# Kernel tuning notes

Hardware: AMD Instinct MI355X
Metric: run time of the kernel (lower is better)

Reference implementation:

```python
import jax, jax.numpy as jnp
import numpy as np

B, L, D = 8, 2048, 10
MIN_INTENSITY = 1e-12


def setup_inputs() -> dict:
    key = jax.random.key(0)
    k1, k2, k3, k4, k5 = jax.random.split(key, 5)
    # strictly increasing event times per sequence in [0, ~100)
    time_points = jnp.sort(jax.random.uniform(k1, (B, L), dtype=jnp.float32) * 100.0, axis=1)
    T = time_points[:, -1] + 1.0  # observation horizon per batch element
    event_types = jax.random.randint(k2, (B, L), 0, D)  # all valid (no -1 padding)
    mu_raw = jax.random.normal(k3, (D,), dtype=jnp.float32)
    log_alpha = jax.random.normal(k4, (D, D), dtype=jnp.float32) - 2.0
    log_beta = jax.random.normal(k5, (D, D), dtype=jnp.float32)
    return {"time_points": time_points, "T": T, "mu_raw": mu_raw,
            "log_alpha": log_alpha, "log_beta": log_beta, "event_types": event_types}


def reference(time_points, T, mu_raw, log_alpha, log_beta, event_types):
    sp = jax.nn.softplus
    mu, alpha, beta = sp(mu_raw), sp(log_alpha), sp(log_beta)  # (D,), (D,D), (D,D)
    e = event_types                      # (B, L)
    valid = e >= 0                       # padding marked with -1
    e_safe = jnp.where(valid, e, 0)

    # ---- positive (event) log-likelihood: O(L^2) pairwise exp-decay sums ----
    td = time_points[:, :, None] - time_points[:, None, :]        # (B, L, L) t_i - t_j
    a = alpha[e_safe[:, :, None], e_safe[:, None, :]]             # (B, L, L)
    b = beta[e_safe[:, :, None], e_safe[:, None, :]]
    expo = jnp.clip(-b * td, -20.0, 0.0)                          # clamp as in source
    inter = a * b * jnp.exp(expo)
    tri = jnp.tril(jnp.ones((L, L), dtype=bool), -1)              # strictly past events
    vmask = valid[:, :, None] & valid[:, None, :]
    inter = jnp.where(tri[None, :, :] & vmask, inter, 0.0)
    lam = mu[e_safe] * valid.astype(mu.dtype) + inter.sum(-1)     # (B, L) intensities
    logl = jnp.where(valid, jnp.log(jnp.clip(lam, MIN_INTENSITY, None)), 0.0)
    pos = logl.sum(-1)                                            # (B,)
    n_valid = valid.sum(-1)
    pos = jnp.where(n_valid == 0, 0.0, pos)

    # ---- compensator: cumulative intensity integral over [0, T] ----
    dt = jnp.where(valid, T[:, None] - time_points, 0.0)          # (B, L)
    ae = alpha[:, e_safe]                                         # (D, B, L)
    be = beta[:, e_safe]
    contrib = ae * (1.0 - jnp.exp(-be * dt[None, :, :]))
    contrib = jnp.where(valid[None, :, :], contrib, 0.0)
    integral = mu[:, None] * T[None, :] + contrib.sum(-1)         # (D, B)

    return pos - integral.sum(0)                                  # (B,) log-likelihood
```

## Files before the change

### kernel.cpp

```cpp
#include <hip/hip_runtime.h>
#include <math.h>

#define NB 8
#define L 2048
#define ND 10
#define NSLICE 32
#define JS 64
#define IT 256
#define TABR 11
#define LOG2E 1.4426950408889634f
#define LN2   0.6931471805599453f
#define CLIP2 (-28.853900817779268f)

#if __has_builtin(__builtin_amdgcn_exp2f)
#define EXP2F(x) __builtin_amdgcn_exp2f(x)
#else
#define EXP2F(x) exp2f(x)
#endif
#if __has_builtin(__builtin_amdgcn_logf)
#define LOGNF(x) (LN2 * __builtin_amdgcn_logf(x))
#else
#define LOGNF(x) logf(x)
#endif

__device__ __forceinline__ float softplus(float x) {
    return (x > 20.0f) ? x : log1pf(expf(x));
}

__global__ __launch_bounds__(256) void hawkes_pairs(
    const float* __restrict__ tp, const int* __restrict__ et,
    const float* __restrict__ la, const float* __restrict__ lb,
    float* __restrict__ part)
{
    __shared__ float2 tab[TABR * ND];
    __shared__ int2   js[JS];
    const int tid = threadIdx.x;

    if (tid < ND * ND) {
        const float a  = softplus(la[tid]);
        const float bb = softplus(lb[tid]);
        const int ei = tid / ND, ej = tid % ND;
        tab[ej * ND + ei] = make_float2(a * bb, bb * LOG2E);
    } else if (tid < ND * ND + ND) {
        tab[ND * ND + (tid - ND * ND)] = make_float2(0.0f, 0.0f);
    }

    const int bx = blockIdx.x;
    const int b  = blockIdx.y;
    int k = 7;
    while (k > 0 && bx < 2 * k * (k + 1)) --k;
    const int s = bx - 2 * k * (k + 1);
    const int jbase = s * JS;
    const int i = k * IT + tid;

    if (tid < JS) {
        const int   ejraw = et[b * L + jbase + tid];
        const float tj    = tp[b * L + jbase + tid];
        const int   ejs   = (ejraw >= 0) ? ejraw : ND;
        js[tid] = make_int2(__float_as_int(tj), ejs * (int)(ND * sizeof(float2)));
    }
    __syncthreads();

    const float ti    = tp[b * L + i];
    const int   eiraw = et[b * L + i];
    const bool  vi    = eiraw >= 0;
    const char* tabp  = (const char*)tab + (vi ? eiraw : 0) * (int)sizeof(float2);

    float acc = 0.0f;
    if (jbase < k * IT) {
        #pragma unroll 16
        for (int jj = 0; jj < JS; ++jj) {
            const int2   q = js[jj];
            const float2 p = *(const float2*)(tabp + q.y);
            const float  x = fmaxf(p.y * (__int_as_float(q.x) - ti), CLIP2);
            acc = fmaf(p.x, EXP2F(x), acc);
        }
    } else {
        #pragma unroll 16
        for (int jj = 0; jj < JS; ++jj) {
            const int2   q = js[jj];
            const float2 p = *(const float2*)(tabp + q.y);
            const float  x = fmaxf(p.y * (__int_as_float(q.x) - ti), CLIP2);
            const float  w = (jbase + jj < i) ? p.x : 0.0f;
            acc = fmaf(w, EXP2F(x), acc);
        }
    }
    part[(b * NSLICE + s) * L + i] = vi ? acc : 0.0f;
}

__global__ __launch_bounds__(256) void hawkes_row(
    const float* __restrict__ tp, const float* __restrict__ Tv,
    const float* __restrict__ mu_raw, const float* __restrict__ la,
    const float* __restrict__ lb, const int* __restrict__ et,
    const float* __restrict__ part, float4* __restrict__ rowred)
{
    __shared__ float aT[ND * ND];
    __shared__ float bT[ND * ND];
    __shared__ float mus[ND];
    __shared__ float rp[4], ri[4];
    __shared__ int   rn[4];

    const int tid  = threadIdx.x;
    const int tile = blockIdx.x;
    const int b    = blockIdx.y;
    if (tid < ND * ND) {
        const int d = tid / ND, c = tid % ND;
        aT[c * ND + d] = softplus(la[tid]);
        bT[c * ND + d] = softplus(lb[tid]) * LOG2E;
    }
    if (tid < ND) mus[tid] = softplus(mu_raw[tid]);
    __syncthreads();

    const int   i    = tile * IT + tid;
    const int   eraw = et[b * L + i];
    const float ti   = tp[b * L + i];
    const bool  v    = eraw >= 0;
    const int   es   = v ? eraw : 0;
    const int   ns   = 4 * (tile + 1);
    const float* pp  = part + b * NSLICE * L + i;

    float lam = v ? mus[es] : 0.0f;
    #pragma unroll
    for (int s0 = 0; s0 < NSLICE; s0 += 4) {
        if (s0 < ns) {
            lam += pp[(s0 + 0) * L];
            lam += pp[(s0 + 1) * L];
            lam += pp[(s0 + 2) * L];
            lam += pp[(s0 + 3) * L];
        }
    }

    float pos = 0.0f, integ = 0.0f;
    int nv = 0;
    if (v) {
        pos = LOGNF(fmaxf(lam, 1e-12f));
        nv = 1;
        const float dt = Tv[b] - ti;
        #pragma unroll
        for (int d2 = 0; d2 < ND; ++d2)
            integ += aT[es * ND + d2] * (1.0f - EXP2F(-bT[es * ND + d2] * dt));
    }
    #pragma unroll
    for (int off = 32; off > 0; off >>= 1) {
        pos   += __shfl_down(pos, off);
        integ += __shfl_down(integ, off);
        nv    += __shfl_down(nv, off);
    }
    const int wid = tid >> 6;
    if ((tid & 63) == 0) { rp[wid] = pos; ri[wid] = integ; rn[wid] = nv; }
    __syncthreads();
    if (tid == 0) {
        rowred[b * 8 + tile] = make_float4(rp[0] + rp[1] + rp[2] + rp[3],
                                           ri[0] + ri[1] + ri[2] + ri[3],
                                           (float)(rn[0] + rn[1] + rn[2] + rn[3]),
                                           0.0f);
    }
}

__global__ void hawkes_out(
    const float* __restrict__ Tv, const float* __restrict__ mu_raw,
    const float4* __restrict__ rowred, float* __restrict__ out)
{
    const int b = threadIdx.x;
    float musum = 0.0f;
    #pragma unroll
    for (int d = 0; d < ND; ++d) musum += softplus(mu_raw[d]);
    if (b < NB) {
        float P = 0.0f, I = 0.0f;
        int   N = 0;
        #pragma unroll
        for (int t = 0; t < 8; ++t) {
            const float4 r = rowred[b * 8 + t];
            P += r.x; I += r.y; N += (int)r.z;
        }
        out[b] = ((N == 0) ? 0.0f : P) - (musum * Tv[b] + I);
    }
}

extern "C" void kernel_launch(void* const* d_in, const int* in_sizes, int n_in,
                              void* d_out, int out_size, void* d_ws, size_t ws_size,
                              hipStream_t stream) {
    const float* tp = (const float*)d_in[0];
    const float* Tv = (const float*)d_in[1];
    const float* mu = (const float*)d_in[2];
    const float* la = (const float*)d_in[3];
    const float* lb = (const float*)d_in[4];
    const int*   et = (const int*)d_in[5];
    float* part = (float*)d_ws;
    float4* rowred = (float4*)(part + (0 * NSLICE + 31) * L);
    float* out = (float*)d_out;

    hipLaunchKernelGGL(hawkes_pairs, dim3(144, NB), dim3(256), 0, stream,
                       tp, et, la, lb, part);
    hipLaunchKernelGGL(hawkes_row, dim3(8, NB), dim3(256), 0, stream,
                       tp, Tv, mu, la, lb, et, part, rowred);
    hipLaunchKernelGGL(hawkes_out, dim3(1), dim3(64), 0, stream,
                       Tv, mu, rowred, out);
}
```

Baseline: 79.37 us.

## Fuse three Hawkes kernels into one with last-block-done atomic counters

Merges the pairwise, per-row and final-output kernels into a single launch. Atomic counters pick the last block per row tile to reduce partial sums, and then the last tile overall to write outputs. This removes two kernel launches and the gaps between them, at the cost of a memset, threadfences and atomics in every block.

```diff
diff --git a/kernel.cpp b/kernel.cpp
--- a/kernel.cpp
+++ b/kernel.cpp
@@ -8,6 +8,8 @@
 #define JS 64
 #define IT 256
 #define TABR 11
+#define BLOCKS_PER_B 144
+#define GRID (NB * BLOCKS_PER_B)
 #define LOG2E 1.4426950408889634f
 #define LN2   0.6931471805599453f
 #define CLIP2 (-28.853900817779268f)
@@ -27,14 +29,31 @@
     return (x > 20.0f) ? x : log1pf(expf(x));
 }
 
-__global__ __launch_bounds__(256) void hawkes_pairs(
-    const float* __restrict__ tp, const int* __restrict__ et,
-    const float* __restrict__ la, const float* __restrict__ lb,
-    float* __restrict__ part)
+__global__ __launch_bounds__(256) void hawkes_one(
+    const float* __restrict__ tp, const float* __restrict__ Tv,
+    const float* __restrict__ mu_raw, const float* __restrict__ la,
+    const float* __restrict__ lb, const int* __restrict__ et,
+    float* __restrict__ part, float4* __restrict__ rowred,
+    int* __restrict__ cntT, int* __restrict__ cntD, float* __restrict__ out)
 {
     __shared__ float2 tab[TABR * ND];
     __shared__ int2   js[JS];
+    __shared__ float  aT[ND * ND];
+    __shared__ float  bT[ND * ND];
+    __shared__ float  mus[ND];
+    __shared__ float  rp[4], ri[4];
+    __shared__ int    rn[4];
+    __shared__ int    win;
+
     const int tid = threadIdx.x;
+    const int bx  = blockIdx.x;
+    const int b   = bx / BLOCKS_PER_B;
+    const int r   = bx - b * BLOCKS_PER_B;
+    int k = 7;
+    while (k > 0 && r < 2 * k * (k + 1)) --k;
+    const int s = r - 2 * k * (k + 1);
+    const int jbase = s * JS;
+    const int i = k * IT + tid;
 
     if (tid < ND * ND) {
         const float a  = softplus(la[tid]);
@@ -44,15 +63,6 @@
     } else if (tid < ND * ND + ND) {
         tab[ND * ND + (tid - ND * ND)] = make_float2(0.0f, 0.0f);
     }
-
-    const int bx = blockIdx.x;
-    const int b  = blockIdx.y;
-    int k = 7;
-    while (k > 0 && bx < 2 * k * (k + 1)) --k;
-    const int s = bx - 2 * k * (k + 1);
-    const int jbase = s * JS;
-    const int i = k * IT + tid;
-
     if (tid < JS) {
         const int   ejraw = et[b * L + jbase + tid];
         const float tj    = tp[b * L + jbase + tid];
@@ -86,23 +96,15 @@
         }
     }
     part[(b * NSLICE + s) * L + i] = vi ? acc : 0.0f;
-}
 
-__global__ __launch_bounds__(256) void hawkes_row(
-    const float* __restrict__ tp, const float* __restrict__ Tv,
-    const float* __restrict__ mu_raw, const float* __restrict__ la,
-    const float* __restrict__ lb, const int* __restrict__ et,
-    const float* __restrict__ part, float4* __restrict__ rowred)
-{
-    __shared__ float aT[ND * ND];
-    __shared__ float bT[ND * ND];
-    __shared__ float mus[ND];
-    __shared__ float rp[4], ri[4];
-    __shared__ int   rn[4];
+    const int nslices = 4 * (k + 1);
+    __threadfence();
+    __syncthreads();
+    if (tid == 0) win = (atomicAdd(&cntT[b * 8 + k], 1) == nslices - 1);
+    __syncthreads();
+    if (!win) return;
+    __threadfence();
 
-    const int tid  = threadIdx.x;
-    const int tile = blockIdx.x;
-    const int b    = blockIdx.y;
     if (tid < ND * ND) {
         const int d = tid / ND, c = tid % ND;
         aT[c * ND + d] = softplus(la[tid]);
@@ -111,18 +113,11 @@
     if (tid < ND) mus[tid] = softplus(mu_raw[tid]);
     __syncthreads();
 
-    const int   i    = tile * IT + tid;
-    const int   eraw = et[b * L + i];
-    const float ti   = tp[b * L + i];
-    const bool  v    = eraw >= 0;
-    const int   es   = v ? eraw : 0;
-    const int   ns   = 4 * (tile + 1);
-    const float* pp  = part + b * NSLICE * L + i;
-
-    float lam = v ? mus[es] : 0.0f;
+    const float* pp = part + b * NSLICE * L + i;
+    float lam = vi ? mus[eiraw] : 0.0f;
     #pragma unroll
     for (int s0 = 0; s0 < NSLICE; s0 += 4) {
-        if (s0 < ns) {
+        if (s0 < nslices) {
             lam += pp[(s0 + 0) * L];
             lam += pp[(s0 + 1) * L];
             lam += pp[(s0 + 2) * L];
@@ -132,13 +127,13 @@
 
     float pos = 0.0f, integ = 0.0f;
     int nv = 0;
-    if (v) {
+    if (vi) {
         pos = LOGNF(fmaxf(lam, 1e-12f));
         nv = 1;
         const float dt = Tv[b] - ti;
         #pragma unroll
         for (int d2 = 0; d2 < ND; ++d2)
-            integ += aT[es * ND + d2] * (1.0f - EXP2F(-bT[es * ND + d2] * dt));
+            integ += aT[eiraw * ND + d2] * (1.0f - EXP2F(-bT[eiraw * ND + d2] * dt));
     }
     #pragma unroll
     for (int off = 32; off > 0; off >>= 1) {
@@ -150,30 +145,31 @@
     if ((tid & 63) == 0) { rp[wid] = pos; ri[wid] = integ; rn[wid] = nv; }
     __syncthreads();
     if (tid == 0) {
-        rowred[b * 8 + tile] = make_float4(rp[0] + rp[1] + rp[2] + rp[3],
-                                           ri[0] + ri[1] + ri[2] + ri[3],
-                                           (float)(rn[0] + rn[1] + rn[2] + rn[3]),
-                                           0.0f);
+        rowred[b * 8 + k] = make_float4(rp[0] + rp[1] + rp[2] + rp[3],
+                                        ri[0] + ri[1] + ri[2] + ri[3],
+                                        (float)(rn[0] + rn[1] + rn[2] + rn[3]),
+                                        0.0f);
     }
-}
 
-__global__ void hawkes_out(
-    const float* __restrict__ Tv, const float* __restrict__ mu_raw,
-    const float4* __restrict__ rowred, float* __restrict__ out)
-{
-    const int b = threadIdx.x;
-    float musum = 0.0f;
-    #pragma unroll
-    for (int d = 0; d < ND; ++d) musum += softplus(mu_raw[d]);
-    if (b < NB) {
+    __threadfence();
+    __syncthreads();
+    if (tid == 0) win = (atomicAdd(cntD, 1) == 63);
+    __syncthreads();
+    if (!win) return;
+    __threadfence();
+
+    if (tid < NB) {
+        float musum = 0.0f;
+        #pragma unroll
+        for (int d = 0; d < ND; ++d) musum += softplus(mu_raw[d]);
         float P = 0.0f, I = 0.0f;
         int   N = 0;
         #pragma unroll
         for (int t = 0; t < 8; ++t) {
-            const float4 r = rowred[b * 8 + t];
-            P += r.x; I += r.y; N += (int)r.z;
+            const float4 rr = rowred[tid * 8 + t];
+            P += rr.x; I += rr.y; N += (int)rr.z;
         }
-        out[b] = ((N == 0) ? 0.0f : P) - (musum * Tv[b] + I);
+        out[tid] = ((N == 0) ? 0.0f : P) - (musum * Tv[tid] + I);
     }
 }
 
@@ -186,14 +182,15 @@
     const float* la = (const float*)d_in[3];
     const float* lb = (const float*)d_in[4];
     const int*   et = (const int*)d_in[5];
-    float* part = (float*)d_ws;
-    float4* rowred = (float4*)(part + (0 * NSLICE + 31) * L);
-    float* out = (float*)d_out;
 
-    hipLaunchKernelGGL(hawkes_pairs, dim3(144, NB), dim3(256), 0, stream,
-                       tp, et, la, lb, part);
-    hipLaunchKernelGGL(hawkes_row, dim3(8, NB), dim3(256), 0, stream,
-                       tp, Tv, mu, la, lb, et, part, rowred);
-    hipLaunchKernelGGL(hawkes_out, dim3(1), dim3(64), 0, stream,
-                       Tv, mu, rowred, out);
+    float*  part   = (float*)d_ws;
+    char*   base   = (char*)d_ws + (size_t)NB * NSLICE * L * 4;
+    float4* rowred = (float4*)base;
+    int*    cntT   = (int*)(base + 1024);
+    int*    cntD   = (int*)(base + 1024 + 256);
+    float*  outp   = (float*)d_out;
+
+    hipMemsetAsync((void*)cntT, 0, 260, stream);
+    hipLaunchKernelGGL(hawkes_one, dim3(GRID), dim3(256), 0, stream,
+                       tp, Tv, mu, la, lb, et, part, rowred, cntT, cntD, outp);
 }
```

Result: slower. 199.6 us (+151.4%).
